# Kernel optimization log

Hardware: AMD Instinct MI355X
Metric: run time of the kernel (lower is better)

The kernel has to match this reference:

```python
import jax, jax.numpy as jnp
import numpy as np

BATCH = 10000
SEQ = 80
VOCAB = 10000
EMB = 100
UNITS = 64


def setup_inputs() -> dict:
    key = jax.random.key(0)
    k1, k2, k3, k4 = jax.random.split(key, 4)
    tokens = jax.random.randint(k1, (BATCH, SEQ), 0, VOCAB)
    emb = jax.random.normal(k2, (VOCAB, EMB), dtype=jnp.float32) * 0.05
    Wx = jax.random.normal(k3, (EMB, UNITS), dtype=jnp.float32) * (1.0 / np.sqrt(EMB))
    Wh = jax.random.normal(k4, (UNITS, UNITS), dtype=jnp.float32) * (1.0 / np.sqrt(UNITS))
    b = jnp.zeros((UNITS,), dtype=jnp.float32)
    Wfc = jax.random.normal(jax.random.fold_in(key, 5), (UNITS, 1), dtype=jnp.float32) * (1.0 / np.sqrt(UNITS))
    bfc = jnp.zeros((1,), dtype=jnp.float32)
    return {"tokens": tokens, "emb": emb, "Wx": Wx, "Wh": Wh, "b": b, "Wfc": Wfc, "bfc": bfc}


def reference(tokens, emb, Wx, Wh, b, Wfc, bfc):
    # Embedding lookup: [B, T, E]
    x = emb[tokens]
    # Precompute input projections for all timesteps: [T, B, U]
    xp = jnp.einsum('bte,eu->tbu', x, Wx) + b
    h0 = jnp.zeros((tokens.shape[0], Wh.shape[0]), dtype=emb.dtype)

    def step(h, xt):
        h_new = jnp.tanh(xt + h @ Wh)  # SimpleRNNCell: tanh(x Wx + h Wh + b)
        return h_new, None

    h_last, _ = jax.lax.scan(step, h0, xp)
    logits = h_last @ Wfc + bfc  # [B, 1]
    return jax.nn.sigmoid(logits)
```

## Files before the change

### kernel.cpp

```cpp
#include <hip/hip_runtime.h>
#include <stdint.h>

#define B_ 10000
#define T_ 80
#define E_ 100
#define U_ 64

typedef __attribute__((ext_vector_type(8))) short bf16x8;
typedef __attribute__((ext_vector_type(4))) float f32x4;

union FragU { bf16x8 v; uint32_t u[4]; short s[8]; };
union LdU  { uint4 q4; bf16x8 v; };

__device__ __forceinline__ void split_bf16(float w, short& hi, short& lo) {
    uint32_t wb  = __float_as_uint(w);
    uint32_t hib = wb & 0xFFFF0000u;
    float rem = w - __uint_as_float(hib);
    hi = (short)(hib >> 16);
    lo = (short)(__float_as_uint(rem) >> 16);
}

__device__ __forceinline__ short bf16_rne(float w) {
    uint32_t u = __float_as_uint(w);
    uint32_t r = (u + 0x7FFFu + ((u >> 16) & 1u)) >> 16;
    return (short)r;
}

__device__ __forceinline__ float tanh_fast(float v) {
    float e  = __expf(2.0f * fabsf(v));
    float r  = __builtin_amdgcn_rcpf(e + 1.0f);
    float tn = fmaf(-2.0f, r, 1.0f);
    uint32_t res = (__float_as_uint(tn) & 0x7FFFFFFFu) | (__float_as_uint(v) & 0x80000000u);
    return __uint_as_float(res);
}

__device__ __forceinline__ float sigmoid_f(float logit) {
    if (logit >= 0.0f) return __builtin_amdgcn_rcpf(1.0f + __expf(-logit));
    float e = __expf(logit);
    return e * __builtin_amdgcn_rcpf(1.0f + e);
}

__device__ __forceinline__ void gather_x(const float* __restrict__ erow, int q, f32x4 xf[7]) {
    #pragma unroll
    for (int kk = 0; kk < 3; ++kk) {
        const int k0 = 8 * q + 32 * kk;
        xf[2 * kk]     = *(const f32x4*)(erow + k0);
        xf[2 * kk + 1] = *(const f32x4*)(erow + k0 + 4);
    }
    xf[6] = *(const f32x4*)(erow + 96);
}

__device__ __forceinline__ void cvt_x(const f32x4 xf[7], FragU ax[4]) {
    #pragma unroll
    for (int kk = 0; kk < 3; ++kk) {
        ax[kk].u[0] = __builtin_amdgcn_perm(__float_as_uint(xf[2*kk][1]),   __float_as_uint(xf[2*kk][0]),   0x07060302u);
        ax[kk].u[1] = __builtin_amdgcn_perm(__float_as_uint(xf[2*kk][3]),   __float_as_uint(xf[2*kk][2]),   0x07060302u);
        ax[kk].u[2] = __builtin_amdgcn_perm(__float_as_uint(xf[2*kk+1][1]), __float_as_uint(xf[2*kk+1][0]), 0x07060302u);
        ax[kk].u[3] = __builtin_amdgcn_perm(__float_as_uint(xf[2*kk+1][3]), __float_as_uint(xf[2*kk+1][2]), 0x07060302u);
    }
    ax[3].u[0] = __builtin_amdgcn_perm(__float_as_uint(xf[6][1]), __float_as_uint(xf[6][0]), 0x07060302u);
    ax[3].u[1] = __builtin_amdgcn_perm(__float_as_uint(xf[6][3]), __float_as_uint(xf[6][2]), 0x07060302u);
    ax[3].u[2] = ax[3].u[0];
    ax[3].u[3] = ax[3].u[1];
}

#define MFMA(A, Bf, C) __builtin_amdgcn_mfma_f32_16x16x32_bf16((A), (Bf), (C), 0, 0, 0)

__global__ __launch_bounds__(64, 1)
void rnn_v9(const int* __restrict__ tokens, const float* __restrict__ emb,
            const float* __restrict__ Wx, const float* __restrict__ Wh,
            const float* __restrict__ bias, const float* __restrict__ Wfc,
            const float* __restrict__ bfc, float* __restrict__ out)
{
    __shared__ __align__(16) unsigned short Hhi[16 * 64];
    __shared__ __align__(16) unsigned short Hlo[16 * 64];
    __shared__ int toks[16 * T_];

    const int l = threadIdx.x;
    const int q = l >> 4, p = l & 15;
    const int R0 = blockIdx.x * 16;

    for (int i = l; i < 16 * T_; i += 64) toks[i] = tokens[R0 * T_ + i];

    FragU wxh[4][4];
    #pragma unroll
    for (int kk = 0; kk < 4; ++kk)
        #pragma unroll
        for (int n = 0; n < 4; ++n)
            #pragma unroll
            for (int j = 0; j < 8; ++j) {
                int k = 8 * q + j + 32 * kk;
                float v = (k < E_) ? Wx[k * U_ + 16 * n + p] : 0.0f;
                wxh[kk][n].s[j] = bf16_rne(v);
            }
    FragU whh[2][4], whl[2][4];
    #pragma unroll
    for (int kk = 0; kk < 2; ++kk)
        #pragma unroll
        for (int n = 0; n < 4; ++n)
            #pragma unroll
            for (int j = 0; j < 8; ++j) {
                float v = Wh[(8 * q + j + 32 * kk) * U_ + 16 * n + p];
                split_bf16(v, whh[kk][n].s[j], whl[kk][n].s[j]);
            }

    float bv[4], wf[4];
    #pragma unroll
    for (int n = 0; n < 4; ++n) { bv[n] = bias[16 * n + p]; wf[n] = Wfc[16 * n + p]; }
    const f32x4 z4 = {0.0f, 0.0f, 0.0f, 0.0f};

    { uint32_t* a = (uint32_t*)Hhi; uint32_t* b = (uint32_t*)Hlo;
      for (int i = l; i < 512; i += 64) { a[i] = 0u; b[i] = 0u; } }

    const int rswz   = (p & 7) << 3;
    const int rdoff0 = p * 64 + ((8 * q)      ^ rswz);
    const int rdoff1 = p * 64 + ((32 + 8 * q) ^ rswz);

    f32x4 X[7];
    FragU ax[4];
    gather_x(emb + (size_t)toks[p * T_ + 0] * E_, q, X);
    cvt_x(X, ax);
    f32x4 P[4];
    #pragma unroll
    for (int n = 0; n < 4; ++n) {
        f32x4 bn = {bv[n], bv[n], bv[n], bv[n]};
        f32x4 c = MFMA(ax[0].v, wxh[0][n].v, bn);
        c = MFMA(ax[1].v, wxh[1][n].v, c);
        c = MFMA(ax[2].v, wxh[2][n].v, c);
        c = MFMA(ax[3].v, wxh[3][n].v, c);
        P[n] = c;
    }
    gather_x(emb + (size_t)toks[p * T_ + 1] * E_, q, X);
    int tokc = toks[p * T_ + 2];

    LdU ah0, ah1, al0, al1;
    ah0.q4 = *(const uint4*)(Hhi + rdoff0);
    ah1.q4 = *(const uint4*)(Hhi + rdoff1);
    al0.q4 = *(const uint4*)(Hlo + rdoff0);
    al1.q4 = *(const uint4*)(Hlo + rdoff1);

    float hl[16];

    for (int t = 0; t < T_; ++t) {
        FragU axn[4];
        cvt_x(X, axn);
        gather_x(emb + (size_t)tokc * E_, q, X);
        int ti = t + 3; if (ti > T_ - 1) ti = T_ - 1;
        const int tokn = toks[p * T_ + ti];

        f32x4 acc[4];
        #pragma unroll
        for (int n = 0; n < 4; ++n) {
            f32x4 c1 = MFMA(ah0.v, whh[0][n].v, P[n]);
            c1       = MFMA(ah1.v, whh[1][n].v, c1);
            f32x4 c2 = MFMA(al0.v, whh[0][n].v, z4);
            c2       = MFMA(al1.v, whh[1][n].v, c2);
            f32x4 c3 = MFMA(ah0.v, whl[0][n].v, z4);
            c3       = MFMA(ah1.v, whl[1][n].v, c3);
            acc[n] = (c1 + c2) + c3;
        }

        #pragma unroll
        for (int r = 0; r < 4; ++r) {
            const int row   = 4 * q + r;
            const int wbase = row * 64;
            const int wswz  = (row & 7) << 3;
            #pragma unroll
            for (int n = 0; n < 4; ++n) {
                float h = tanh_fast(acc[n][r]);
                hl[r * 4 + n] = h;
                uint32_t hb  = __float_as_uint(h);
                uint32_t hib = hb & 0xFFFF0000u;
                float rem = h - __uint_as_float(hib);
                const int idx = wbase + ((16 * n + p) ^ wswz);
                Hhi[idx] = (unsigned short)(hb >> 16);
                Hlo[idx] = (unsigned short)(__float_as_uint(rem) >> 16);
            }
        }

        ah0.q4 = *(const uint4*)(Hhi + rdoff0);
        ah1.q4 = *(const uint4*)(Hhi + rdoff1);
        al0.q4 = *(const uint4*)(Hlo + rdoff0);
        al1.q4 = *(const uint4*)(Hlo + rdoff1);

        #pragma unroll
        for (int n = 0; n < 4; ++n) {
            f32x4 bn = {bv[n], bv[n], bv[n], bv[n]};
            f32x4 c = MFMA(axn[0].v, wxh[0][n].v, bn);
            c = MFMA(axn[1].v, wxh[1][n].v, c);
            c = MFMA(axn[2].v, wxh[2][n].v, c);
            c = MFMA(axn[3].v, wxh[3][n].v, c);
            P[n] = c;
        }
        tokc = tokn;
    }

    #pragma unroll
    for (int r = 0; r < 4; ++r) {
        float part = hl[r * 4 + 0] * wf[0] + hl[r * 4 + 1] * wf[1]
                   + hl[r * 4 + 2] * wf[2] + hl[r * 4 + 3] * wf[3];
        part += __shfl_xor(part, 1);
        part += __shfl_xor(part, 2);
        part += __shfl_xor(part, 4);
        part += __shfl_xor(part, 8);
        if (p == 0) out[R0 + 4 * q + r] = sigmoid_f(part + bfc[0]);
    }
}

extern "C" void kernel_launch(void* const* d_in, const int* in_sizes, int n_in,
                              void* d_out, int out_size, void* d_ws, size_t ws_size,
                              hipStream_t stream) {
    const int*   tokens = (const int*)  d_in[0];
    const float* emb    = (const float*)d_in[1];
    const float* Wx     = (const float*)d_in[2];
    const float* Wh     = (const float*)d_in[3];
    const float* b      = (const float*)d_in[4];
    const float* Wfc    = (const float*)d_in[5];
    const float* bfc    = (const float*)d_in[6];
    float* out          = (float*)d_out;

    rnn_v9<<<B_ / 16, 64, 0, stream>>>(tokens, emb, Wx, Wh, b, Wfc, bfc, out);
}
```

Before: 144.6 us.

## Interleave two independent 16-row RNN tiles per wave to hide latency

Each 64-thread block now carries two independent 16-row batch tiles (A and B) through the recurrence, interleaving their MFMA, tanh, LDS and gather phases. The point is to hide the serial MFMA/LDS dependency latency of one tile behind work from the other, with the grid halved to 313 blocks. The Wh correction MFMAs are also merged into one accumulator chain. The cost is higher register pressure and fewer blocks (313 vs 625) across the CUs, which may underfill the machine.

```diff
diff --git a/kernel.cpp b/kernel.cpp
--- a/kernel.cpp
+++ b/kernel.cpp
@@ -67,20 +67,26 @@
 #define MFMA(A, Bf, C) __builtin_amdgcn_mfma_f32_16x16x32_bf16((A), (Bf), (C), 0, 0, 0)
 
 __global__ __launch_bounds__(64, 1)
-void rnn_v9(const int* __restrict__ tokens, const float* __restrict__ emb,
-            const float* __restrict__ Wx, const float* __restrict__ Wh,
-            const float* __restrict__ bias, const float* __restrict__ Wfc,
-            const float* __restrict__ bfc, float* __restrict__ out)
+void rnn_v10(const int* __restrict__ tokens, const float* __restrict__ emb,
+             const float* __restrict__ Wx, const float* __restrict__ Wh,
+             const float* __restrict__ bias, const float* __restrict__ Wfc,
+             const float* __restrict__ bfc, float* __restrict__ out)
 {
-    __shared__ __align__(16) unsigned short Hhi[16 * 64];
-    __shared__ __align__(16) unsigned short Hlo[16 * 64];
-    __shared__ int toks[16 * T_];
+    __shared__ __align__(16) unsigned short HhiA[16 * 64], HloA[16 * 64];
+    __shared__ __align__(16) unsigned short HhiB[16 * 64], HloB[16 * 64];
+    __shared__ int toksA[16 * T_], toksB[16 * T_];
 
     const int l = threadIdx.x;
     const int q = l >> 4, p = l & 15;
-    const int R0 = blockIdx.x * 16;
-
-    for (int i = l; i < 16 * T_; i += 64) toks[i] = tokens[R0 * T_ + i];
+    const int R0A = blockIdx.x * 32;
+    const int R0B_real = R0A + 16;
+    const bool haveB = (R0B_real + 16) <= B_;
+    const int R0B = haveB ? R0B_real : R0A;
+
+    for (int i = l; i < 16 * T_; i += 64) {
+        toksA[i] = tokens[R0A * T_ + i];
+        toksB[i] = tokens[R0B * T_ + i];
+    }
 
     FragU wxh[4][4];
     #pragma unroll
@@ -109,101 +115,141 @@
     for (int n = 0; n < 4; ++n) { bv[n] = bias[16 * n + p]; wf[n] = Wfc[16 * n + p]; }
     const f32x4 z4 = {0.0f, 0.0f, 0.0f, 0.0f};
 
-    { uint32_t* a = (uint32_t*)Hhi; uint32_t* b = (uint32_t*)Hlo;
-      for (int i = l; i < 512; i += 64) { a[i] = 0u; b[i] = 0u; } }
+    { uint32_t* a0 = (uint32_t*)HhiA; uint32_t* a1 = (uint32_t*)HloA;
+      uint32_t* b0 = (uint32_t*)HhiB; uint32_t* b1 = (uint32_t*)HloB;
+      for (int i = l; i < 512; i += 64) { a0[i]=0u; a1[i]=0u; b0[i]=0u; b1[i]=0u; } }
 
     const int rswz   = (p & 7) << 3;
     const int rdoff0 = p * 64 + ((8 * q)      ^ rswz);
     const int rdoff1 = p * 64 + ((32 + 8 * q) ^ rswz);
 
-    f32x4 X[7];
-    FragU ax[4];
-    gather_x(emb + (size_t)toks[p * T_ + 0] * E_, q, X);
-    cvt_x(X, ax);
-    f32x4 P[4];
-    #pragma unroll
-    for (int n = 0; n < 4; ++n) {
-        f32x4 bn = {bv[n], bv[n], bv[n], bv[n]};
-        f32x4 c = MFMA(ax[0].v, wxh[0][n].v, bn);
-        c = MFMA(ax[1].v, wxh[1][n].v, c);
-        c = MFMA(ax[2].v, wxh[2][n].v, c);
-        c = MFMA(ax[3].v, wxh[3][n].v, c);
-        P[n] = c;
-    }
-    gather_x(emb + (size_t)toks[p * T_ + 1] * E_, q, X);
-    int tokc = toks[p * T_ + 2];
-
-    LdU ah0, ah1, al0, al1;
-    ah0.q4 = *(const uint4*)(Hhi + rdoff0);
-    ah1.q4 = *(const uint4*)(Hhi + rdoff1);
-    al0.q4 = *(const uint4*)(Hlo + rdoff0);
-    al1.q4 = *(const uint4*)(Hlo + rdoff1);
-
-    float hl[16];
-
-    for (int t = 0; t < T_; ++t) {
-        FragU axn[4];
-        cvt_x(X, axn);
-        gather_x(emb + (size_t)tokc * E_, q, X);
-        int ti = t + 3; if (ti > T_ - 1) ti = T_ - 1;
-        const int tokn = toks[p * T_ + ti];
-
-        f32x4 acc[4];
-        #pragma unroll
-        for (int n = 0; n < 4; ++n) {
-            f32x4 c1 = MFMA(ah0.v, whh[0][n].v, P[n]);
-            c1       = MFMA(ah1.v, whh[1][n].v, c1);
-            f32x4 c2 = MFMA(al0.v, whh[0][n].v, z4);
-            c2       = MFMA(al1.v, whh[1][n].v, c2);
-            f32x4 c3 = MFMA(ah0.v, whl[0][n].v, z4);
-            c3       = MFMA(ah1.v, whl[1][n].v, c3);
-            acc[n] = (c1 + c2) + c3;
-        }
-
-        #pragma unroll
-        for (int r = 0; r < 4; ++r) {
-            const int row   = 4 * q + r;
-            const int wbase = row * 64;
-            const int wswz  = (row & 7) << 3;
-            #pragma unroll
-            for (int n = 0; n < 4; ++n) {
-                float h = tanh_fast(acc[n][r]);
-                hl[r * 4 + n] = h;
-                uint32_t hb  = __float_as_uint(h);
-                uint32_t hib = hb & 0xFFFF0000u;
-                float rem = h - __uint_as_float(hib);
-                const int idx = wbase + ((16 * n + p) ^ wswz);
-                Hhi[idx] = (unsigned short)(hb >> 16);
-                Hlo[idx] = (unsigned short)(__float_as_uint(rem) >> 16);
-            }
-        }
-
-        ah0.q4 = *(const uint4*)(Hhi + rdoff0);
-        ah1.q4 = *(const uint4*)(Hhi + rdoff1);
-        al0.q4 = *(const uint4*)(Hlo + rdoff0);
-        al1.q4 = *(const uint4*)(Hlo + rdoff1);
-
+    f32x4 XA[7], XB[7];
+    f32x4 PA[4], PB[4];
+    int tokcA, tokcB;
+    {
+        FragU ax[4];
+        gather_x(emb + (size_t)toksA[p * T_ + 0] * E_, q, XA);
+        gather_x(emb + (size_t)toksB[p * T_ + 0] * E_, q, XB);
+        cvt_x(XA, ax);
         #pragma unroll
         for (int n = 0; n < 4; ++n) {
             f32x4 bn = {bv[n], bv[n], bv[n], bv[n]};
-            f32x4 c = MFMA(axn[0].v, wxh[0][n].v, bn);
-            c = MFMA(axn[1].v, wxh[1][n].v, c);
-            c = MFMA(axn[2].v, wxh[2][n].v, c);
-            c = MFMA(axn[3].v, wxh[3][n].v, c);
-            P[n] = c;
+            f32x4 c = MFMA(ax[0].v, wxh[0][n].v, bn);
+            c = MFMA(ax[1].v, wxh[1][n].v, c);
+            c = MFMA(ax[2].v, wxh[2][n].v, c);
+            c = MFMA(ax[3].v, wxh[3][n].v, c);
+            PA[n] = c;
         }
-        tokc = tokn;
-    }
+        cvt_x(XB, ax);
+        #pragma unroll
+        for (int n = 0; n < 4; ++n) {
+            f32x4 bn = {bv[n], bv[n], bv[n], bv[n]};
+            f32x4 c = MFMA(ax[0].v, wxh[0][n].v, bn);
+            c = MFMA(ax[1].v, wxh[1][n].v, c);
+            c = MFMA(ax[2].v, wxh[2][n].v, c);
+            c = MFMA(ax[3].v, wxh[3][n].v, c);
+            PB[n] = c;
+        }
+        gather_x(emb + (size_t)toksA[p * T_ + 1] * E_, q, XA);
+        gather_x(emb + (size_t)toksB[p * T_ + 1] * E_, q, XB);
+        tokcA = toksA[p * T_ + 2];
+        tokcB = toksB[p * T_ + 2];
+    }
+
+    LdU ah0A, ah1A, al0A, al1A, ah0B, ah1B, al0B, al1B;
+    ah0A.q4 = *(const uint4*)(HhiA + rdoff0);  ah1A.q4 = *(const uint4*)(HhiA + rdoff1);
+    al0A.q4 = *(const uint4*)(HloA + rdoff0);  al1A.q4 = *(const uint4*)(HloA + rdoff1);
+    ah0B.q4 = *(const uint4*)(HhiB + rdoff0);  ah1B.q4 = *(const uint4*)(HhiB + rdoff1);
+    al0B.q4 = *(const uint4*)(HloB + rdoff0);  al1B.q4 = *(const uint4*)(HloB + rdoff1);
+
+    float hlA[16], hlB[16];
+
+#define PH_CVT(S)                                                                  \
+    FragU axn##S[4];                                                               \
+    cvt_x(X##S, axn##S);                                                           \
+    gather_x(emb + (size_t)tokc##S * E_, q, X##S);                                 \
+    { int ti = t + 3; if (ti > T_ - 1) ti = T_ - 1; tokc##S = toks##S[p * T_ + ti]; }
+
+#define PH_REC(S)                                                                  \
+    f32x4 acc##S[4];                                                               \
+    _Pragma("unroll")                                                              \
+    for (int n = 0; n < 4; ++n) {                                                  \
+        f32x4 c1 = MFMA(ah0##S.v, whh[0][n].v, P##S[n]);                           \
+        c1       = MFMA(ah1##S.v, whh[1][n].v, c1);                                \
+        f32x4 c2 = MFMA(al0##S.v, whh[0][n].v, z4);                                \
+        c2       = MFMA(al1##S.v, whh[1][n].v, c2);                                \
+        c2       = MFMA(ah0##S.v, whl[0][n].v, c2);                                \
+        c2       = MFMA(ah1##S.v, whl[1][n].v, c2);                                \
+        acc##S[n] = c1 + c2;                                                       \
+    }
+
+#define PH_TANH(S)                                                                 \
+    _Pragma("unroll")                                                              \
+    for (int r = 0; r < 4; ++r) {                                                  \
+        const int row   = 4 * q + r;                                               \
+        const int wbase = row * 64;                                                \
+        const int wswz  = (row & 7) << 3;                                          \
+        _Pragma("unroll")                                                          \
+        for (int n = 0; n < 4; ++n) {                                              \
+            float h = tanh_fast(acc##S[n][r]);                                     \
+            hl##S[r * 4 + n] = h;                                                  \
+            uint32_t hb  = __float_as_uint(h);                                     \
+            uint32_t hib = hb & 0xFFFF0000u;                                       \
+            float rem = h - __uint_as_float(hib);                                  \
+            const int idx = wbase + ((16 * n + p) ^ wswz);                         \
+            Hhi##S[idx] = (unsigned short)(hb >> 16);                              \
+            Hlo##S[idx] = (unsigned short)(__float_as_uint(rem) >> 16);            \
+        }                                                                          \
+    }
+
+#define PH_READ(S)                                                                 \
+    ah0##S.q4 = *(const uint4*)(Hhi##S + rdoff0);                                  \
+    ah1##S.q4 = *(const uint4*)(Hhi##S + rdoff1);                                  \
+    al0##S.q4 = *(const uint4*)(Hlo##S + rdoff0);                                  \
+    al1##S.q4 = *(const uint4*)(Hlo##S + rdoff1);
+
+#define PH_PROJ(S)                                                                 \
+    _Pragma("unroll")                                                              \
+    for (int n = 0; n < 4; ++n) {                                                  \
+        f32x4 bn = {bv[n], bv[n], bv[n], bv[n]};                                   \
+        f32x4 c = MFMA(axn##S[0].v, wxh[0][n].v, bn);                              \
+        c = MFMA(axn##S[1].v, wxh[1][n].v, c);                                     \
+        c = MFMA(axn##S[2].v, wxh[2][n].v, c);                                     \
+        c = MFMA(axn##S[3].v, wxh[3][n].v, c);                                     \
+        P##S[n] = c;                                                               \
+    }
+
+    for (int t = 0; t < T_; ++t) {
+        PH_CVT(A)  PH_CVT(B)
+        PH_REC(A)  PH_REC(B)
+        PH_TANH(A) PH_TANH(B)
+        PH_READ(A) PH_READ(B)
+        PH_PROJ(A) PH_PROJ(B)
+    }
+#undef PH_CVT
+#undef PH_REC
+#undef PH_TANH
+#undef PH_READ
+#undef PH_PROJ
 
     #pragma unroll
     for (int r = 0; r < 4; ++r) {
-        float part = hl[r * 4 + 0] * wf[0] + hl[r * 4 + 1] * wf[1]
-                   + hl[r * 4 + 2] * wf[2] + hl[r * 4 + 3] * wf[3];
-        part += __shfl_xor(part, 1);
-        part += __shfl_xor(part, 2);
-        part += __shfl_xor(part, 4);
-        part += __shfl_xor(part, 8);
-        if (p == 0) out[R0 + 4 * q + r] = sigmoid_f(part + bfc[0]);
+        float pa = hlA[r * 4 + 0] * wf[0] + hlA[r * 4 + 1] * wf[1]
+                 + hlA[r * 4 + 2] * wf[2] + hlA[r * 4 + 3] * wf[3];
+        pa += __shfl_xor(pa, 1);
+        pa += __shfl_xor(pa, 2);
+        pa += __shfl_xor(pa, 4);
+        pa += __shfl_xor(pa, 8);
+        float pb = hlB[r * 4 + 0] * wf[0] + hlB[r * 4 + 1] * wf[1]
+                 + hlB[r * 4 + 2] * wf[2] + hlB[r * 4 + 3] * wf[3];
+        pb += __shfl_xor(pb, 1);
+        pb += __shfl_xor(pb, 2);
+        pb += __shfl_xor(pb, 4);
+        pb += __shfl_xor(pb, 8);
+        if (p == 0) {
+            out[R0A + 4 * q + r] = sigmoid_f(pa + bfc[0]);
+            if (haveB) out[R0B_real + 4 * q + r] = sigmoid_f(pb + bfc[0]);
+        }
     }
 }
 
@@ -219,5 +265,6 @@
     const float* bfc    = (const float*)d_in[6];
     float* out          = (float*)d_out;
 
-    rnn_v9<<<B_ / 16, 64, 0, stream>>>(tokens, emb, Wx, Wh, b, Wfc, bfc, out);
-}
+    const int grid = (B_ + 31) / 32;
+    rnn_v10<<<grid, 64, 0, stream>>>(tokens, emb, Wx, Wh, b, Wfc, bfc, out);
+}
```

Result: slower. 249.7 us (+72.7%).

## Drop low-half hidden state, keep hi/lo weights, chain MFMAs serially

Applied to the files above, without the earlier changes.

Stores the recurrent hidden state as a single rounded bf16 value instead of a hi/lo split, which halves the LDS writes and reads per step and removes the h_lo x W_hi MFMAs, leaving 4 chained MFMAs per output tile instead of 6 in three chains. The tanh is simplified to a version without the abs and sign fix-up. The hidden state is zero-initialised in registers rather than LDS, and the final tanh is recomputed from the accumulators instead of being kept in an extra register array. This trades accuracy of the recurrent product, with error that can compound over 80 steps, and a longer serial MFMA dependency chain for fewer instructions on the critical path.

```diff
diff --git a/kernel.cpp b/kernel.cpp
--- a/kernel.cpp
+++ b/kernel.cpp
@@ -20,18 +20,16 @@
     lo = (short)(__float_as_uint(rem) >> 16);
 }
 
-__device__ __forceinline__ short bf16_rne(float w) {
+__device__ __forceinline__ unsigned short bf16_rne(float w) {
     uint32_t u = __float_as_uint(w);
     uint32_t r = (u + 0x7FFFu + ((u >> 16) & 1u)) >> 16;
-    return (short)r;
-}
-
-__device__ __forceinline__ float tanh_fast(float v) {
-    float e  = __expf(2.0f * fabsf(v));
-    float r  = __builtin_amdgcn_rcpf(e + 1.0f);
-    float tn = fmaf(-2.0f, r, 1.0f);
-    uint32_t res = (__float_as_uint(tn) & 0x7FFFFFFFu) | (__float_as_uint(v) & 0x80000000u);
-    return __uint_as_float(res);
+    return (unsigned short)r;
+}
+
+__device__ __forceinline__ float tanh_fast5(float v) {
+    float e = __expf(2.0f * v);
+    float r = __builtin_amdgcn_rcpf(e + 1.0f);
+    return fmaf(-2.0f, r, 1.0f);
 }
 
 __device__ __forceinline__ float sigmoid_f(float logit) {
@@ -67,13 +65,12 @@
 #define MFMA(A, Bf, C) __builtin_amdgcn_mfma_f32_16x16x32_bf16((A), (Bf), (C), 0, 0, 0)
 
 __global__ __launch_bounds__(64, 1)
-void rnn_v9(const int* __restrict__ tokens, const float* __restrict__ emb,
-            const float* __restrict__ Wx, const float* __restrict__ Wh,
-            const float* __restrict__ bias, const float* __restrict__ Wfc,
-            const float* __restrict__ bfc, float* __restrict__ out)
+void rnn_v11(const int* __restrict__ tokens, const float* __restrict__ emb,
+             const float* __restrict__ Wx, const float* __restrict__ Wh,
+             const float* __restrict__ bias, const float* __restrict__ Wfc,
+             const float* __restrict__ bfc, float* __restrict__ out)
 {
-    __shared__ __align__(16) unsigned short Hhi[16 * 64];
-    __shared__ __align__(16) unsigned short Hlo[16 * 64];
+    __shared__ __align__(16) unsigned short Hq[16 * 64];
     __shared__ int toks[16 * T_];
 
     const int l = threadIdx.x;
@@ -91,7 +88,7 @@
             for (int j = 0; j < 8; ++j) {
                 int k = 8 * q + j + 32 * kk;
                 float v = (k < E_) ? Wx[k * U_ + 16 * n + p] : 0.0f;
-                wxh[kk][n].s[j] = bf16_rne(v);
+                wxh[kk][n].s[j] = (short)bf16_rne(v);
             }
     FragU whh[2][4], whl[2][4];
     #pragma unroll
@@ -107,39 +104,35 @@
     float bv[4], wf[4];
     #pragma unroll
     for (int n = 0; n < 4; ++n) { bv[n] = bias[16 * n + p]; wf[n] = Wfc[16 * n + p]; }
-    const f32x4 z4 = {0.0f, 0.0f, 0.0f, 0.0f};
-
-    { uint32_t* a = (uint32_t*)Hhi; uint32_t* b = (uint32_t*)Hlo;
-      for (int i = l; i < 512; i += 64) { a[i] = 0u; b[i] = 0u; } }
 
     const int rswz   = (p & 7) << 3;
     const int rdoff0 = p * 64 + ((8 * q)      ^ rswz);
     const int rdoff1 = p * 64 + ((32 + 8 * q) ^ rswz);
 
     f32x4 X[7];
-    FragU ax[4];
-    gather_x(emb + (size_t)toks[p * T_ + 0] * E_, q, X);
-    cvt_x(X, ax);
     f32x4 P[4];
-    #pragma unroll
-    for (int n = 0; n < 4; ++n) {
-        f32x4 bn = {bv[n], bv[n], bv[n], bv[n]};
-        f32x4 c = MFMA(ax[0].v, wxh[0][n].v, bn);
-        c = MFMA(ax[1].v, wxh[1][n].v, c);
-        c = MFMA(ax[2].v, wxh[2][n].v, c);
-        c = MFMA(ax[3].v, wxh[3][n].v, c);
-        P[n] = c;
-    }
-    gather_x(emb + (size_t)toks[p * T_ + 1] * E_, q, X);
+    {
+        FragU ax[4];
+        gather_x(emb + (size_t)toks[p * T_ + 0] * E_, q, X);
+        cvt_x(X, ax);
+        #pragma unroll
+        for (int n = 0; n < 4; ++n) {
+            f32x4 bn = {bv[n], bv[n], bv[n], bv[n]};
+            f32x4 c = MFMA(ax[0].v, wxh[0][n].v, bn);
+            c = MFMA(ax[1].v, wxh[1][n].v, c);
+            c = MFMA(ax[2].v, wxh[2][n].v, c);
+            c = MFMA(ax[3].v, wxh[3][n].v, c);
+            P[n] = c;
+        }
+        gather_x(emb + (size_t)toks[p * T_ + 1] * E_, q, X);
+    }
     int tokc = toks[p * T_ + 2];
 
-    LdU ah0, ah1, al0, al1;
-    ah0.q4 = *(const uint4*)(Hhi + rdoff0);
-    ah1.q4 = *(const uint4*)(Hhi + rdoff1);
-    al0.q4 = *(const uint4*)(Hlo + rdoff0);
-    al1.q4 = *(const uint4*)(Hlo + rdoff1);
-
-    float hl[16];
+    LdU ah0, ah1;
+    ah0.q4 = (uint4){0, 0, 0, 0};
+    ah1.q4 = (uint4){0, 0, 0, 0};
+
+    f32x4 acc[4];
 
     for (int t = 0; t < T_; ++t) {
         FragU axn[4];
@@ -148,16 +141,13 @@
         int ti = t + 3; if (ti > T_ - 1) ti = T_ - 1;
         const int tokn = toks[p * T_ + ti];
 
-        f32x4 acc[4];
         #pragma unroll
         for (int n = 0; n < 4; ++n) {
-            f32x4 c1 = MFMA(ah0.v, whh[0][n].v, P[n]);
-            c1       = MFMA(ah1.v, whh[1][n].v, c1);
-            f32x4 c2 = MFMA(al0.v, whh[0][n].v, z4);
-            c2       = MFMA(al1.v, whh[1][n].v, c2);
-            f32x4 c3 = MFMA(ah0.v, whl[0][n].v, z4);
-            c3       = MFMA(ah1.v, whl[1][n].v, c3);
-            acc[n] = (c1 + c2) + c3;
+            f32x4 c = MFMA(ah0.v, whh[0][n].v, P[n]);
+            c = MFMA(ah1.v, whh[1][n].v, c);
+            c = MFMA(ah0.v, whl[0][n].v, c);
+            c = MFMA(ah1.v, whl[1][n].v, c);
+            acc[n] = c;
         }
 
         #pragma unroll
@@ -167,21 +157,13 @@
             const int wswz  = (row & 7) << 3;
             #pragma unroll
             for (int n = 0; n < 4; ++n) {
-                float h = tanh_fast(acc[n][r]);
-                hl[r * 4 + n] = h;
-                uint32_t hb  = __float_as_uint(h);
-                uint32_t hib = hb & 0xFFFF0000u;
-                float rem = h - __uint_as_float(hib);
-                const int idx = wbase + ((16 * n + p) ^ wswz);
-                Hhi[idx] = (unsigned short)(hb >> 16);
-                Hlo[idx] = (unsigned short)(__float_as_uint(rem) >> 16);
+                float h = tanh_fast5(acc[n][r]);
+                Hq[wbase + ((16 * n + p) ^ wswz)] = bf16_rne(h);
             }
         }
 
-        ah0.q4 = *(const uint4*)(Hhi + rdoff0);
-        ah1.q4 = *(const uint4*)(Hhi + rdoff1);
-        al0.q4 = *(const uint4*)(Hlo + rdoff0);
-        al1.q4 = *(const uint4*)(Hlo + rdoff1);
+        ah0.q4 = *(const uint4*)(Hq + rdoff0);
+        ah1.q4 = *(const uint4*)(Hq + rdoff1);
 
         #pragma unroll
         for (int n = 0; n < 4; ++n) {
@@ -197,8 +179,8 @@
 
     #pragma unroll
     for (int r = 0; r < 4; ++r) {
-        float part = hl[r * 4 + 0] * wf[0] + hl[r * 4 + 1] * wf[1]
-                   + hl[r * 4 + 2] * wf[2] + hl[r * 4 + 3] * wf[3];
+        float part = tanh_fast5(acc[0][r]) * wf[0] + tanh_fast5(acc[1][r]) * wf[1]
+                   + tanh_fast5(acc[2][r]) * wf[2] + tanh_fast5(acc[3][r]) * wf[3];
         part += __shfl_xor(part, 1);
         part += __shfl_xor(part, 2);
         part += __shfl_xor(part, 4);
@@ -219,5 +201,5 @@
     const float* bfc    = (const float*)d_in[6];
     float* out          = (float*)d_out;
 
-    rnn_v9<<<B_ / 16, 64, 0, stream>>>(tokens, emb, Wx, Wh, b, Wfc, bfc, out);
-}
+    rnn_v11<<<B_ / 16, 64, 0, stream>>>(tokens, emb, Wx, Wh, b, Wfc, bfc, out);
+}
```

Measured after the change: 128.2 us. 1.13x faster.
